# Kernel optimization log

Measured on AMD Instinct MI355X. Metric: run time of the kernel, lower is better.

Reference implementation:

```python
import jax, jax.numpy as jnp
import numpy as np

T, D, H, E, K = 4096, 1024, 2816, 8, 2


def setup_inputs() -> dict:
    key = jax.random.key(0)
    ks = jax.random.split(key, 5)
    s = 0.02
    return {
        "x": jax.random.normal(ks[0], (T, D), dtype=jnp.float32),
        "gate_w": jax.random.normal(ks[1], (D, E), dtype=jnp.float32) * s,
        "w1": jax.random.normal(ks[2], (E, D, H), dtype=jnp.float32) * s,
        "w2": jax.random.normal(ks[3], (E, H, D), dtype=jnp.float32) * s,
        "w3": jax.random.normal(ks[4], (E, D, H), dtype=jnp.float32) * s,
    }


def reference(x, gate_w, w1, w2, w3):
    # gate + top-k routing
    gate_logits = x @ gate_w                          # [T, E]
    topk_vals, sel = jax.lax.top_k(gate_logits, K)    # [T, K]
    topk_w = jax.nn.softmax(topk_vals.astype(jnp.float32), axis=-1).astype(x.dtype)
    # scatter top-k weights back to a dense [T, E] combine matrix
    tok = jnp.arange(x.shape[0])[:, None]             # [T, 1]
    combine = jnp.zeros(gate_logits.shape, x.dtype).at[tok, sel].set(topk_w)  # [T, E]
    # per-expert SwiGLU FFN, evaluated densely and combined with (mostly-zero) weights;
    # mathematically identical to the masked gather/scatter loop in the original.
    h = jax.nn.silu(jnp.einsum("td,edh->teh", x, w1)) * jnp.einsum("td,edh->teh", x, w3)
    expert_out = jnp.einsum("teh,ehd->ted", h, w2)    # [T, E, D]
    return jnp.einsum("ted,te->td", expert_out, combine)
```

## Files before the change

### kernel.cpp

```cpp
#include <hip/hip_runtime.h>
#include <hip/hip_bf16.h>
#include <cstdint>
#include <cstddef>


#define Tt 4096
#define Dd 1024
#define Hh 2816
#define Ee 8
#define NVT 71
#define NTILE 5632
#define FFN1_BLKS ((Hh / 128) * NVT)

typedef __bf16 bf16_t;
typedef __bf16 bf16x4 __attribute__((ext_vector_type(4)));
typedef __bf16 bf16x8 __attribute__((ext_vector_type(8)));
typedef float f32x4 __attribute__((ext_vector_type(4)));

__device__ __forceinline__ void gload16(const void* g, void* l) {
  __builtin_amdgcn_global_load_lds(
      (__attribute__((address_space(1))) void*)(void*)(uintptr_t)g,
      (__attribute__((address_space(3))) void*)l, 16, 0, 0);
}
#define WAIT_VM0() asm volatile("s_waitcnt vmcnt(0)" ::: "memory")

__device__ __forceinline__ void prep_tile(const float* __restrict__ src,
                                          bf16_t* __restrict__ dst, int R, int C,
                                          int tbid, bf16_t* tile, int tid) {
  const int tilesC = C / 64, tilesR = R / 64;
  const int e = tbid / (tilesR * tilesC);
  const int rem = tbid % (tilesR * tilesC);
  const int r0 = (rem / tilesC) * 64, c0 = (rem % tilesC) * 64;
  src += (size_t)e * R * C;
  dst += (size_t)e * R * C;
  const int rr0 = tid >> 4;
  const int c4 = (tid & 15) * 4;
#pragma unroll
  for (int i = 0; i < 4; ++i) {
    const int r = rr0 + i * 16;
    const float4 v = *(const float4*)(src + (size_t)(r0 + r) * C + c0 + c4);
    tile[(c4 + 0) * 68 + r] = (__bf16)v.x;
    tile[(c4 + 1) * 68 + r] = (__bf16)v.y;
    tile[(c4 + 2) * 68 + r] = (__bf16)v.z;
    tile[(c4 + 3) * 68 + r] = (__bf16)v.w;
  }
  __syncthreads();
  const int rch = (tid & 7) * 8;
#pragma unroll
  for (int i = 0; i < 2; ++i) {
    const int c = (tid >> 3) + i * 32;
    const uint2 lo = *(const uint2*)(tile + c * 68 + rch);
    const uint2 hi = *(const uint2*)(tile + c * 68 + rch + 4);
    uint4 val; val.x = lo.x; val.y = lo.y; val.z = hi.x; val.w = hi.y;
    *(uint4*)(dst + (size_t)(c0 + c) * R + r0 + rch) = val;
  }
}

__global__ __launch_bounds__(256) void gate_prep13_kernel(
    const float* __restrict__ x, const float* __restrict__ gw_g,
    const float* __restrict__ w1, const float* __restrict__ w3,
    int* __restrict__ counts, int* __restrict__ perm, float* __restrict__ topkw,
    bf16_t* __restrict__ xb, bf16_t* __restrict__ w1t, bf16_t* __restrict__ w3t) {
  __shared__ __align__(16) char smem[Dd * 9 * 4];
  const int tid = threadIdx.x;
  const int bid = blockIdx.x;
  if (bid >= 128) {
    const int pbid = bid - 128;
    bf16_t* tile = (bf16_t*)smem;
    if (pbid < NTILE) prep_tile(w1, w1t, Dd, Hh, pbid, tile, tid);
    else prep_tile(w3, w3t, Dd, Hh, pbid - NTILE, tile, tid);
    return;
  }
  float* gw = (float*)smem;
  for (int i = tid; i < Dd * Ee; i += 256) gw[(i >> 3) * 9 + (i & 7)] = gw_g[i];
  __syncthreads();
  const int tok = bid * 32 + (tid >> 3);
  const int part = tid & 7;
  const float* xr = x + (size_t)tok * Dd;
  float acc[Ee];
#pragma unroll
  for (int e = 0; e < Ee; ++e) acc[e] = 0.f;
  for (int i = 0; i < 32; ++i) {
    const int d = i * 32 + part * 4;
    const float4 xv = *(const float4*)(xr + d);
    bf16x4 bv; bv[0] = (__bf16)xv.x; bv[1] = (__bf16)xv.y; bv[2] = (__bf16)xv.z; bv[3] = (__bf16)xv.w;
    *(bf16x4*)(xb + (size_t)tok * Dd + d) = bv;
    const float xs[4] = {xv.x, xv.y, xv.z, xv.w};
#pragma unroll
    for (int j = 0; j < 4; ++j)
#pragma unroll
      for (int e = 0; e < Ee; ++e) acc[e] += xs[j] * gw[(d + j) * 9 + e];
  }
#pragma unroll
  for (int s = 1; s < 8; s <<= 1)
#pragma unroll
    for (int e = 0; e < Ee; ++e) acc[e] += __shfl_xor(acc[e], s, 64);
  if (part == 0) {
    int i0 = 0; float v0 = acc[0];
#pragma unroll
    for (int e = 1; e < Ee; ++e) if (acc[e] > v0) { v0 = acc[e]; i0 = e; }
    int i1 = -1; float v1 = -1e30f;
#pragma unroll
    for (int e = 0; e < Ee; ++e)
      if (e != i0 && acc[e] > v1) { v1 = acc[e]; i1 = e; }
    const float w0 = 1.f / (1.f + __expf(v1 - v0));
    topkw[tok * 2 + 0] = w0;
    topkw[tok * 2 + 1] = 1.f - w0;
    const int p0 = atomicAdd(&counts[i0], 1);
    perm[i0 * Tt + p0] = tok * 2 + 0;
    const int p1 = atomicAdd(&counts[i1], 1);
    perm[i1 * Tt + p1] = tok * 2 + 1;
  }
}

__global__ void scan_kernel(const int* __restrict__ counts, int* __restrict__ offs,
                            int* __restrict__ ts) {
  if (threadIdx.x == 0) {
    int s = 0, t = 0;
    for (int e = 0; e < Ee; ++e) {
      offs[e] = s; ts[e] = t;
      s += counts[e]; t += (counts[e] + 127) >> 7;
    }
    offs[Ee] = s; ts[Ee] = t;
  }
}

__global__ __launch_bounds__(256, 2) void ffn1_prep2_kernel(
    const bf16_t* __restrict__ xb, const bf16_t* __restrict__ w1t,
    const bf16_t* __restrict__ w3t, const float* __restrict__ w2,
    const int* __restrict__ perm, const int* __restrict__ counts,
    const int* __restrict__ offs, const int* __restrict__ ts,
    bf16_t* __restrict__ hbuf, bf16_t* __restrict__ w2t) {
  __shared__ __align__(16) char smem[3 * 128 * 64 * 2];
  const int tid = threadIdx.x;
  const int obid = blockIdx.x;
  if (obid >= FFN1_BLKS) {
    prep_tile(w2, w2t, Hh, Dd, obid - FFN1_BLKS, (bf16_t*)smem, tid);
    return;
  }
  bf16_t* As = (bf16_t*)smem;
  bf16_t* B1s = As + 128 * 64;
  bf16_t* B3s = B1s + 128 * 64;

  const int G = FFN1_BLKS;
  const int xcd = obid & 7, seq = obid >> 3;
  const int q = G >> 3, r = G & 7;
  const int lin = (xcd < r ? xcd * (q + 1) : r * (q + 1) + (xcd - r) * q) + seq;
  const int vt = lin % NVT;
  const int nb = lin / NVT;
  if (vt >= ts[Ee]) return;
  int e = 0;
#pragma unroll
  for (int i = 1; i < Ee; ++i) if (vt >= ts[i]) e = i;
  const int ne = counts[e];
  const int m0 = (vt - ts[e]) * 128;
  const int h0 = nb * 128;
  const int hb = offs[e];

  const int lane = tid & 63;
  const int wid = tid >> 6;

  const int scol = ((tid & 7) << 3) ^ (((tid >> 3) & 7) << 3);
  uint32_t aoff[4], boff[4];
#pragma unroll
  for (int i = 0; i < 4; ++i) {
    const int row = i * 32 + (tid >> 3);
    const int gr = m0 + row;
    const int rec = (gr < ne) ? perm[e * Tt + gr] : 0;
    aoff[i] = (uint32_t)((rec >> 1) * Dd + scol);
    boff[i] = (uint32_t)((h0 + row) * Dd + scol);
  }
  const bf16_t* w1e = w1t + (size_t)e * Hh * Dd;
  const bf16_t* w3e = w3t + (size_t)e * Hh * Dd;

  f32x4 acc1[4][4], acc3[4][4];
#pragma unroll
  for (int m = 0; m < 4; ++m)
#pragma unroll
    for (int n = 0; n < 4; ++n) {
      acc1[m][n] = (f32x4){0.f, 0.f, 0.f, 0.f};
      acc3[m][n] = (f32x4){0.f, 0.f, 0.f, 0.f};
    }

  const int wm = wid >> 1, wn = wid & 1;
  int aoffm[4], boffn[4], koff[2];
#pragma unroll
  for (int m = 0; m < 4; ++m) aoffm[m] = (wm * 64 + m * 16 + (lane & 15)) * 64;
#pragma unroll
  for (int n = 0; n < 4; ++n) boffn[n] = (wn * 64 + n * 16 + (lane & 15)) * 64;
#pragma unroll
  for (int kk = 0; kk < 2; ++kk)
    koff[kk] = (kk * 32 + (lane >> 4) * 8) ^ ((lane & 7) << 3);

  for (int kt = 0; kt < Dd / 64; ++kt) {
    const int d0 = kt * 64;
    __syncthreads();
#pragma unroll
    for (int i = 0; i < 4; ++i) {
      const int lb = (i * 256 + tid) * 8;
      gload16(xb + aoff[i] + d0, As + lb);
      gload16(w1e + boff[i] + d0, B1s + lb);
      gload16(w3e + boff[i] + d0, B3s + lb);
    }
    WAIT_VM0();
    __syncthreads();
#pragma unroll
    for (int kk = 0; kk < 2; ++kk) {
      bf16x8 a[4], b1[4], b3[4];
#pragma unroll
      for (int m = 0; m < 4; ++m) a[m] = *(const bf16x8*)(As + aoffm[m] + koff[kk]);
#pragma unroll
      for (int n = 0; n < 4; ++n) {
        b1[n] = *(const bf16x8*)(B1s + boffn[n] + koff[kk]);
        b3[n] = *(const bf16x8*)(B3s + boffn[n] + koff[kk]);
      }
#pragma unroll
      for (int m = 0; m < 4; ++m)
#pragma unroll
        for (int n = 0; n < 4; ++n) {
          acc1[m][n] = __builtin_amdgcn_mfma_f32_16x16x32_bf16(a[m], b1[n], acc1[m][n], 0, 0, 0);
          acc3[m][n] = __builtin_amdgcn_mfma_f32_16x16x32_bf16(a[m], b3[n], acc3[m][n], 0, 0, 0);
        }
    }
  }

#pragma unroll
  for (int m = 0; m < 4; ++m) {
    const int rb = m0 + wm * 64 + m * 16 + ((lane >> 4) << 2);
#pragma unroll
    for (int r2 = 0; r2 < 4; ++r2) {
      const int gr = rb + r2;
      if (gr >= ne) continue;
      bf16_t* orow = hbuf + (size_t)(hb + gr) * Hh + h0 + wn * 64 + (lane & 15);
#pragma unroll
      for (int n = 0; n < 4; ++n) {
        const float v1 = acc1[m][n][r2];
        const float v3 = acc3[m][n][r2];
        const float s = v1 / (1.f + __expf(-v1));
        orow[n * 16] = (__bf16)(s * v3);
      }
    }
  }
}

__global__ __launch_bounds__(256, 3) void ffn2_kernel(
    const bf16_t* __restrict__ hbuf, const bf16_t* __restrict__ w2t,
    const int* __restrict__ perm, const int* __restrict__ counts,
    const int* __restrict__ offs, const int* __restrict__ ts,
    const float* __restrict__ topkw, float* __restrict__ obuf) {
  const int G = (Dd / 128) * NVT;
  const int orig = blockIdx.x;
  const int xcd = orig & 7, seq = orig >> 3;
  const int q = G >> 3, r = G & 7;
  const int lin = (xcd < r ? xcd * (q + 1) : r * (q + 1) + (xcd - r) * q) + seq;
  const int vt = lin % NVT;
  const int nb = lin / NVT;
  if (vt >= ts[Ee]) return;
  int e = 0;
#pragma unroll
  for (int i = 1; i < Ee; ++i) if (vt >= ts[i]) e = i;
  const int ne = counts[e];
  const int m0 = (vt - ts[e]) * 128;
  const int n0 = nb * 128;
  const int hb = offs[e];

  __shared__ __align__(16) bf16_t As[128 * 64];
  __shared__ __align__(16) bf16_t Bs[128 * 64];

  const int tid = threadIdx.x;
  const int lane = tid & 63;
  const int wid = tid >> 6;
  const int scol = ((tid & 7) << 3) ^ (((tid >> 3) & 7) << 3);
  uint32_t aoff[4], boff[4];
#pragma unroll
  for (int i = 0; i < 4; ++i) {
    const int row = i * 32 + (tid >> 3);
    int ar = hb + m0 + row;
    if (ar > 2 * Tt - 1) ar = 2 * Tt - 1;
    aoff[i] = (uint32_t)(ar * Hh + scol);
    boff[i] = (uint32_t)((n0 + row) * Hh + scol);
  }
  const bf16_t* w2e = w2t + (size_t)e * Dd * Hh;

  f32x4 acc[4][4];
#pragma unroll
  for (int m = 0; m < 4; ++m)
#pragma unroll
    for (int n = 0; n < 4; ++n) acc[m][n] = (f32x4){0.f, 0.f, 0.f, 0.f};

  const int wm = wid >> 1, wn = wid & 1;
  int aoffm[4], boffn[4], koff[2];
#pragma unroll
  for (int m = 0; m < 4; ++m) aoffm[m] = (wm * 64 + m * 16 + (lane & 15)) * 64;
#pragma unroll
  for (int n = 0; n < 4; ++n) boffn[n] = (wn * 64 + n * 16 + (lane & 15)) * 64;
#pragma unroll
  for (int kk = 0; kk < 2; ++kk)
    koff[kk] = (kk * 32 + (lane >> 4) * 8) ^ ((lane & 7) << 3);

  for (int kt = 0; kt < Hh / 64; ++kt) {
    const int k0 = kt * 64;
    __syncthreads();
#pragma unroll
    for (int i = 0; i < 4; ++i) {
      const int lb = (i * 256 + tid) * 8;
      gload16(hbuf + aoff[i] + k0, As + lb);
      gload16(w2e + boff[i] + k0, Bs + lb);
    }
    WAIT_VM0();
    __syncthreads();
#pragma unroll
    for (int kk = 0; kk < 2; ++kk) {
      bf16x8 a[4], b[4];
#pragma unroll
      for (int m = 0; m < 4; ++m) a[m] = *(const bf16x8*)(As + aoffm[m] + koff[kk]);
#pragma unroll
      for (int n = 0; n < 4; ++n) b[n] = *(const bf16x8*)(Bs + boffn[n] + koff[kk]);
#pragma unroll
      for (int m = 0; m < 4; ++m)
#pragma unroll
        for (int n = 0; n < 4; ++n)
          acc[m][n] = __builtin_amdgcn_mfma_f32_16x16x32_bf16(a[m], b[n], acc[m][n], 0, 0, 0);
    }
  }

#pragma unroll
  for (int m = 0; m < 4; ++m) {
    const int rb = m0 + wm * 64 + m * 16 + ((lane >> 4) << 2);
#pragma unroll
    for (int r2 = 0; r2 < 4; ++r2) {
      const int gr = rb + r2;
      if (gr >= ne) continue;
      const int rec = perm[e * Tt + gr];
      const float wgt = topkw[rec];
      float* orow = obuf + (size_t)rec * Dd + n0 + wn * 64 + (lane & 15);
#pragma unroll
      for (int n = 0; n < 4; ++n) orow[n * 16] = wgt * acc[m][n][r2];
    }
  }
}

__global__ __launch_bounds__(256) void combine_kernel(const float* __restrict__ obuf,
                                                      float* __restrict__ out) {
  const int t = blockIdx.x;
  const int d = threadIdx.x * 4;
  const float4 a = *(const float4*)(obuf + (size_t)(2 * t) * Dd + d);
  const float4 b = *(const float4*)(obuf + (size_t)(2 * t + 1) * Dd + d);
  float4 o;
  o.x = a.x + b.x; o.y = a.y + b.y; o.z = a.z + b.z; o.w = a.w + b.w;
  *(float4*)(out + (size_t)t * Dd + d) = o;
}

extern "C" void kernel_launch(void* const* d_in, const int* in_sizes, int n_in,
                              void* d_out, int out_size, void* d_ws, size_t ws_size,
                              hipStream_t stream) {
  const float* x = (const float*)d_in[0];
  const float* gate_w = (const float*)d_in[1];
  const float* w1 = (const float*)d_in[2];
  const float* w2 = (const float*)d_in[3];
  const float* w3 = (const float*)d_in[4];
  float* out = (float*)d_out;

  char* ws = (char*)d_ws;
  size_t off = 0;
  auto alloc = [&](size_t b) { size_t r = off; off += (b + 255) & ~(size_t)255; return r; };
  float* topkw   = (float*)(ws + alloc((size_t)Tt * 2 * 4));
  int* counts    = (int*)(ws + alloc(Ee * 4));
  int* offs      = (int*)(ws + alloc((Ee + 1) * 4));
  int* ts        = (int*)(ws + alloc((Ee + 1) * 4));
  int* perm      = (int*)(ws + alloc((size_t)Ee * Tt * 4));
  bf16_t* xb     = (bf16_t*)(ws + alloc((size_t)Tt * Dd * 2));
  const size_t w1t_off = alloc((size_t)Ee * Hh * Dd * 2);
  bf16_t* w1t    = (bf16_t*)(ws + w1t_off);
  bf16_t* w3t    = (bf16_t*)(ws + alloc((size_t)Ee * Hh * Dd * 2));
  bf16_t* w2t    = (bf16_t*)(ws + alloc((size_t)Ee * Dd * Hh * 2));
  bf16_t* hbuf   = (bf16_t*)(ws + alloc((size_t)Tt * 2 * Hh * 2));
  float* obuf    = (float*)(ws + w1t_off);
  if (ws_size < off) return;

  hipMemsetAsync(counts, 0, Ee * 4, stream);
  gate_prep13_kernel<<<128 + 2 * NTILE, 256, 0, stream>>>(
      x, gate_w, w1, w3, counts, perm, topkw, xb, w1t, w3t);
  scan_kernel<<<1, 64, 0, stream>>>(counts, offs, ts);
  ffn1_prep2_kernel<<<FFN1_BLKS + NTILE, 256, 0, stream>>>(
      xb, w1t, w3t, w2, perm, counts, offs, ts, hbuf, w2t);
  ffn2_kernel<<<(Dd / 128) * NVT, 256, 0, stream>>>(hbuf, w2t, perm, counts, offs, ts, topkw, obuf);
  combine_kernel<<<Tt, 256, 0, stream>>>(obuf, out);
}
```

Baseline: 294.6 us.

## Transpose weights in registers and fuse combine via atomic adds

Replaces the LDS-staged transpose in weight prep with a per-thread 4x4 register transpose, removing shared memory and a barrier from the prep blocks. Drops the separate combine kernel: ffn2 now atomically adds weighted expert outputs directly into a zeroed output. This removes the obuf write/read and one launch, at the cost of fp32 atomics, an extra memset, less-coalesced 8-byte transposed stores, and nondeterministic summation order.

Result: slower. 315.8 us (+7.2%).

```diff
diff --git a/kernel.cpp b/kernel.cpp
--- a/kernel.cpp
+++ b/kernel.cpp
@@ -26,33 +26,25 @@
 
 __device__ __forceinline__ void prep_tile(const float* __restrict__ src,
                                           bf16_t* __restrict__ dst, int R, int C,
-                                          int tbid, bf16_t* tile, int tid) {
+                                          int tbid, int tid) {
   const int tilesC = C / 64, tilesR = R / 64;
   const int e = tbid / (tilesR * tilesC);
   const int rem = tbid % (tilesR * tilesC);
   const int r0 = (rem / tilesC) * 64, c0 = (rem % tilesC) * 64;
-  src += (size_t)e * R * C;
-  dst += (size_t)e * R * C;
-  const int rr0 = tid >> 4;
-  const int c4 = (tid & 15) * 4;
-#pragma unroll
-  for (int i = 0; i < 4; ++i) {
-    const int r = rr0 + i * 16;
-    const float4 v = *(const float4*)(src + (size_t)(r0 + r) * C + c0 + c4);
-    tile[(c4 + 0) * 68 + r] = (__bf16)v.x;
-    tile[(c4 + 1) * 68 + r] = (__bf16)v.y;
-    tile[(c4 + 2) * 68 + r] = (__bf16)v.z;
-    tile[(c4 + 3) * 68 + r] = (__bf16)v.w;
-  }
-  __syncthreads();
-  const int rch = (tid & 7) * 8;
-#pragma unroll
-  for (int i = 0; i < 2; ++i) {
-    const int c = (tid >> 3) + i * 32;
-    const uint2 lo = *(const uint2*)(tile + c * 68 + rch);
-    const uint2 hi = *(const uint2*)(tile + c * 68 + rch + 4);
-    uint4 val; val.x = lo.x; val.y = lo.y; val.z = hi.x; val.w = hi.y;
-    *(uint4*)(dst + (size_t)(c0 + c) * R + r0 + rch) = val;
+  src += (size_t)e * R * C + (size_t)r0 * C + c0;
+  dst += (size_t)e * R * C + (size_t)c0 * R + r0;
+  const int tr = (tid & 15) * 4;
+  const int tc = (tid >> 4) * 4;
+  f32x4 v[4];
+#pragma unroll
+  for (int j = 0; j < 4; ++j)
+    v[j] = *(const f32x4*)(src + (size_t)(tr + j) * C + tc);
+#pragma unroll
+  for (int k = 0; k < 4; ++k) {
+    bf16x4 w;
+    w[0] = (__bf16)v[0][k]; w[1] = (__bf16)v[1][k];
+    w[2] = (__bf16)v[2][k]; w[3] = (__bf16)v[3][k];
+    *(bf16x4*)(dst + (size_t)(tc + k) * R + tr) = w;
   }
 }
 
@@ -61,17 +53,15 @@
     const float* __restrict__ w1, const float* __restrict__ w3,
     int* __restrict__ counts, int* __restrict__ perm, float* __restrict__ topkw,
     bf16_t* __restrict__ xb, bf16_t* __restrict__ w1t, bf16_t* __restrict__ w3t) {
-  __shared__ __align__(16) char smem[Dd * 9 * 4];
   const int tid = threadIdx.x;
   const int bid = blockIdx.x;
   if (bid >= 128) {
     const int pbid = bid - 128;
-    bf16_t* tile = (bf16_t*)smem;
-    if (pbid < NTILE) prep_tile(w1, w1t, Dd, Hh, pbid, tile, tid);
-    else prep_tile(w3, w3t, Dd, Hh, pbid - NTILE, tile, tid);
+    if (pbid < NTILE) prep_tile(w1, w1t, Dd, Hh, pbid, tid);
+    else prep_tile(w3, w3t, Dd, Hh, pbid - NTILE, tid);
     return;
   }
-  float* gw = (float*)smem;
+  __shared__ float gw[Dd * 9];
   for (int i = tid; i < Dd * Ee; i += 256) gw[(i >> 3) * 9 + (i & 7)] = gw_g[i];
   __syncthreads();
   const int tok = bid * 32 + (tid >> 3);
@@ -131,16 +121,15 @@
     const int* __restrict__ perm, const int* __restrict__ counts,
     const int* __restrict__ offs, const int* __restrict__ ts,
     bf16_t* __restrict__ hbuf, bf16_t* __restrict__ w2t) {
-  __shared__ __align__(16) char smem[3 * 128 * 64 * 2];
   const int tid = threadIdx.x;
   const int obid = blockIdx.x;
   if (obid >= FFN1_BLKS) {
-    prep_tile(w2, w2t, Hh, Dd, obid - FFN1_BLKS, (bf16_t*)smem, tid);
+    prep_tile(w2, w2t, Hh, Dd, obid - FFN1_BLKS, tid);
     return;
   }
-  bf16_t* As = (bf16_t*)smem;
-  bf16_t* B1s = As + 128 * 64;
-  bf16_t* B3s = B1s + 128 * 64;
+  __shared__ __align__(16) bf16_t As[128 * 64];
+  __shared__ __align__(16) bf16_t B1s[128 * 64];
+  __shared__ __align__(16) bf16_t B3s[128 * 64];
 
   const int G = FFN1_BLKS;
   const int xcd = obid & 7, seq = obid >> 3;
@@ -247,7 +236,7 @@
     const bf16_t* __restrict__ hbuf, const bf16_t* __restrict__ w2t,
     const int* __restrict__ perm, const int* __restrict__ counts,
     const int* __restrict__ offs, const int* __restrict__ ts,
-    const float* __restrict__ topkw, float* __restrict__ obuf) {
+    const float* __restrict__ topkw, float* __restrict__ out) {
   const int G = (Dd / 128) * NVT;
   const int orig = blockIdx.x;
   const int xcd = orig & 7, seq = orig >> 3;
@@ -333,22 +322,11 @@
       if (gr >= ne) continue;
       const int rec = perm[e * Tt + gr];
       const float wgt = topkw[rec];
-      float* orow = obuf + (size_t)rec * Dd + n0 + wn * 64 + (lane & 15);
-#pragma unroll
-      for (int n = 0; n < 4; ++n) orow[n * 16] = wgt * acc[m][n][r2];
-    }
-  }
-}
-
-__global__ __launch_bounds__(256) void combine_kernel(const float* __restrict__ obuf,
-                                                      float* __restrict__ out) {
-  const int t = blockIdx.x;
-  const int d = threadIdx.x * 4;
-  const float4 a = *(const float4*)(obuf + (size_t)(2 * t) * Dd + d);
-  const float4 b = *(const float4*)(obuf + (size_t)(2 * t + 1) * Dd + d);
-  float4 o;
-  o.x = a.x + b.x; o.y = a.y + b.y; o.z = a.z + b.z; o.w = a.w + b.w;
-  *(float4*)(out + (size_t)t * Dd + d) = o;
+      float* orow = out + (size_t)(rec >> 1) * Dd + n0 + wn * 64 + (lane & 15);
+#pragma unroll
+      for (int n = 0; n < 4; ++n) atomicAdd(&orow[n * 16], wgt * acc[m][n][r2]);
+    }
+  }
 }
 
 extern "C" void kernel_launch(void* const* d_in, const int* in_sizes, int n_in,
@@ -370,20 +348,18 @@
   int* ts        = (int*)(ws + alloc((Ee + 1) * 4));
   int* perm      = (int*)(ws + alloc((size_t)Ee * Tt * 4));
   bf16_t* xb     = (bf16_t*)(ws + alloc((size_t)Tt * Dd * 2));
-  const size_t w1t_off = alloc((size_t)Ee * Hh * Dd * 2);
-  bf16_t* w1t    = (bf16_t*)(ws + w1t_off);
+  bf16_t* w1t    = (bf16_t*)(ws + alloc((size_t)Ee * Hh * Dd * 2));
   bf16_t* w3t    = (bf16_t*)(ws + alloc((size_t)Ee * Hh * Dd * 2));
   bf16_t* w2t    = (bf16_t*)(ws + alloc((size_t)Ee * Dd * Hh * 2));
   bf16_t* hbuf   = (bf16_t*)(ws + alloc((size_t)Tt * 2 * Hh * 2));
-  float* obuf    = (float*)(ws + w1t_off);
   if (ws_size < off) return;
 
   hipMemsetAsync(counts, 0, Ee * 4, stream);
+  hipMemsetAsync(out, 0, (size_t)out_size * 4, stream);
   gate_prep13_kernel<<<128 + 2 * NTILE, 256, 0, stream>>>(
       x, gate_w, w1, w3, counts, perm, topkw, xb, w1t, w3t);
   scan_kernel<<<1, 64, 0, stream>>>(counts, offs, ts);
   ffn1_prep2_kernel<<<FFN1_BLKS + NTILE, 256, 0, stream>>>(
       xb, w1t, w3t, w2, perm, counts, offs, ts, hbuf, w2t);
-  ffn2_kernel<<<(Dd / 128) * NVT, 256, 0, stream>>>(hbuf, w2t, perm, counts, offs, ts, topkw, obuf);
-  combine_kernel<<<Tt, 256, 0, stream>>>(obuf, out);
-}
+  ffn2_kernel<<<(Dd / 128) * NVT, 256, 0, stream>>>(hbuf, w2t, perm, counts, offs, ts, topkw, out);
+}
```

## Split ffn2 K dimension in two and sum partial slices in combine

Applied to the files above, without the earlier changes.

The down-projection kernel now launches twice as many blocks, each covering half of the hidden dimension, and writes weighted partials into one of two separate output slices. The combine kernel sums four partial rows per token instead of two. This is meant to fill the GPU better, since the previous grid was under one wave. In exchange it doubles the fp32 intermediate traffic, and the larger buffer now overlaps the w3t workspace region.

New measurement: 299.2 us. About the same (+1.5%).

```diff
diff --git a/kernel.cpp b/kernel.cpp
--- a/kernel.cpp
+++ b/kernel.cpp
@@ -247,14 +247,15 @@
     const bf16_t* __restrict__ hbuf, const bf16_t* __restrict__ w2t,
     const int* __restrict__ perm, const int* __restrict__ counts,
     const int* __restrict__ offs, const int* __restrict__ ts,
-    const float* __restrict__ topkw, float* __restrict__ obuf) {
-  const int G = (Dd / 128) * NVT;
+    const float* __restrict__ topkw, float* __restrict__ obuf2) {
+  const int G = (Dd / 128) * NVT * 2;
   const int orig = blockIdx.x;
   const int xcd = orig & 7, seq = orig >> 3;
   const int q = G >> 3, r = G & 7;
   const int lin = (xcd < r ? xcd * (q + 1) : r * (q + 1) + (xcd - r) * q) + seq;
   const int vt = lin % NVT;
-  const int nb = lin / NVT;
+  const int nb = (lin / NVT) & 7;
+  const int ks = lin / (NVT * 8);
   if (vt >= ts[Ee]) return;
   int e = 0;
 #pragma unroll
@@ -298,8 +299,10 @@
   for (int kk = 0; kk < 2; ++kk)
     koff[kk] = (kk * 32 + (lane >> 4) * 8) ^ ((lane & 7) << 3);
 
-  for (int kt = 0; kt < Hh / 64; ++kt) {
-    const int k0 = kt * 64;
+  const int nt = (Hh / 64) / 2;
+  const int kbase = ks * nt;
+  for (int kt = 0; kt < nt; ++kt) {
+    const int k0 = (kbase + kt) * 64;
     __syncthreads();
 #pragma unroll
     for (int i = 0; i < 4; ++i) {
@@ -324,6 +327,7 @@
     }
   }
 
+  float* oslice = obuf2 + (size_t)ks * 2 * Tt * Dd;
 #pragma unroll
   for (int m = 0; m < 4; ++m) {
     const int rb = m0 + wm * 64 + m * 16 + ((lane >> 4) << 2);
@@ -333,21 +337,26 @@
       if (gr >= ne) continue;
       const int rec = perm[e * Tt + gr];
       const float wgt = topkw[rec];
-      float* orow = obuf + (size_t)rec * Dd + n0 + wn * 64 + (lane & 15);
+      float* orow = oslice + (size_t)rec * Dd + n0 + wn * 64 + (lane & 15);
 #pragma unroll
       for (int n = 0; n < 4; ++n) orow[n * 16] = wgt * acc[m][n][r2];
     }
   }
 }
 
-__global__ __launch_bounds__(256) void combine_kernel(const float* __restrict__ obuf,
+__global__ __launch_bounds__(256) void combine_kernel(const float* __restrict__ obuf2,
                                                       float* __restrict__ out) {
   const int t = blockIdx.x;
   const int d = threadIdx.x * 4;
-  const float4 a = *(const float4*)(obuf + (size_t)(2 * t) * Dd + d);
-  const float4 b = *(const float4*)(obuf + (size_t)(2 * t + 1) * Dd + d);
+  const float* s0 = obuf2;
+  const float* s1 = obuf2 + (size_t)2 * Tt * Dd;
+  const float4 a = *(const float4*)(s0 + (size_t)(2 * t) * Dd + d);
+  const float4 b = *(const float4*)(s0 + (size_t)(2 * t + 1) * Dd + d);
+  const float4 c = *(const float4*)(s1 + (size_t)(2 * t) * Dd + d);
+  const float4 e = *(const float4*)(s1 + (size_t)(2 * t + 1) * Dd + d);
   float4 o;
-  o.x = a.x + b.x; o.y = a.y + b.y; o.z = a.z + b.z; o.w = a.w + b.w;
+  o.x = a.x + b.x + c.x + e.x; o.y = a.y + b.y + c.y + e.y;
+  o.z = a.z + b.z + c.z + e.z; o.w = a.w + b.w + c.w + e.w;
   *(float4*)(out + (size_t)t * Dd + d) = o;
 }
 
@@ -375,7 +384,7 @@
   bf16_t* w3t    = (bf16_t*)(ws + alloc((size_t)Ee * Hh * Dd * 2));
   bf16_t* w2t    = (bf16_t*)(ws + alloc((size_t)Ee * Dd * Hh * 2));
   bf16_t* hbuf   = (bf16_t*)(ws + alloc((size_t)Tt * 2 * Hh * 2));
-  float* obuf    = (float*)(ws + w1t_off);
+  float* obuf2   = (float*)(ws + w1t_off);
   if (ws_size < off) return;
 
   hipMemsetAsync(counts, 0, Ee * 4, stream);
@@ -384,6 +393,7 @@
   scan_kernel<<<1, 64, 0, stream>>>(counts, offs, ts);
   ffn1_prep2_kernel<<<FFN1_BLKS + NTILE, 256, 0, stream>>>(
       xb, w1t, w3t, w2, perm, counts, offs, ts, hbuf, w2t);
-  ffn2_kernel<<<(Dd / 128) * NVT, 256, 0, stream>>>(hbuf, w2t, perm, counts, offs, ts, topkw, obuf);
-  combine_kernel<<<Tt, 256, 0, stream>>>(obuf, out);
-}
+  ffn2_kernel<<<(Dd / 128) * NVT * 2, 256, 0, stream>>>(
+      hbuf, w2t, perm, counts, offs, ts, topkw, obuf2);
+  combine_kernel<<<Tt, 256, 0, stream>>>(obuf2, out);
+}
```
